# Kernel optimization log

Measured on AMD Instinct MI355X. Metric: run time of the kernel, lower is better.

Reference implementation:

```python
import jax, jax.numpy as jnp
import numpy as np

NMS_THRESHOLD = 0.4
TOP_K = 1000
MAX_BOXES = 300
N_ANCHORS = 300000
N_CLASSES = 80
DET_DIM = 85


def setup_inputs() -> dict:
    key = jax.random.key(0)
    k1, k2, k3, k4 = jax.random.split(key, 4)
    # valid [y1, x1, y2, x2] boxes: top-left corner + positive height/width
    yx = jax.random.uniform(k1, (1, N_ANCHORS, 2), jnp.float32) * 512.0
    hw = jax.random.uniform(k2, (1, N_ANCHORS, 2), jnp.float32) * 64.0 + 1.0
    boxes = jnp.concatenate([yx, yx + hw], axis=-1)
    classification = jax.random.uniform(k3, (1, N_ANCHORS, N_CLASSES), jnp.float32)
    detections = jax.random.normal(k4, (1, N_ANCHORS, DET_DIM), jnp.float32)
    return {"boxes": boxes, "classification": classification, "detections": detections}


def _iou_matrix(b):
    # b: [K, 4] as [y1, x1, y2, x2]
    y1, x1, y2, x2 = b[:, 0], b[:, 1], b[:, 2], b[:, 3]
    area = (y2 - y1) * (x2 - x1)
    ih = jnp.clip(jnp.minimum(y2[:, None], y2[None, :]) - jnp.maximum(y1[:, None], y1[None, :]), 0.0)
    iw = jnp.clip(jnp.minimum(x2[:, None], x2[None, :]) - jnp.maximum(x1[:, None], x1[None, :]), 0.0)
    inter = ih * iw
    return inter / (area[:, None] + area[None, :] - inter + 1e-8)


def _nms_forward(boxes, classification, detections):
    b = boxes[0]                      # [N, 4]
    cls = classification[0]           # [N, C]
    det = detections[0]               # [N, D]
    scores = jnp.max(cls, axis=1)     # [N]
    # pre-NMS top-k filter (lax.top_k returns scores sorted descending)
    _, idx = jax.lax.top_k(scores, TOP_K)
    b_k = b[idx]                      # [K, 4]
    det_k = det[idx]                  # [K, D]
    iou = _iou_matrix(b_k)            # [K, K]
    # greedy NMS over score-sorted candidates: keep box i iff no higher-scoring
    # kept box overlaps it above the threshold
    def step(keep, i):
        suppressed = jnp.any(keep & (iou[i] > NMS_THRESHOLD))
        return keep.at[i].set(~suppressed), None
    keep, _ = jax.lax.scan(step, jnp.zeros(TOP_K, dtype=bool), jnp.arange(TOP_K))
    # first MAX_BOXES kept candidates (in score order), zero-padded
    pos = jnp.where(keep, jnp.arange(TOP_K), TOP_K)
    pos = jnp.sort(pos)[:MAX_BOXES]
    valid = pos < TOP_K
    sel = det_k[jnp.minimum(pos, TOP_K - 1)]          # [MAX_BOXES, D]
    out = jnp.where(valid[:, None], sel, 0.0)
    return out[None]                   # [1, MAX_BOXES, D]


def reference(boxes, classification, detections):
    return _nms_forward(boxes, classification, detections)
```

## Files before the change

### kernel.cpp

```cpp
#include <hip/hip_runtime.h>
#include <stdint.h>

#define N_ANCH   300000
#define N_CLS    80
#define DET_DIM  85
#define TOPK     1000
#define MAXB     300
#define NMS_THR  0.4f
#define CAP      4096
#define NBH      32
#define N4       (N_ANCH / 4)
#define ITH      ((N4 + NBH*1024 - 1) / (NBH*1024))

#define OFF_SBITS   0
#define OFF_HA      300032
#define OFF_HB      304128
#define OFF_META    308224
#define OFF_CAND    308288
#define OFF_TOPK    316480
#define OFF_BOXK    317480
#define OFF_MASK    321480

__device__ __forceinline__ void gridbar(uint32_t* bar, uint32_t target) {
    __syncthreads();
    if (threadIdx.x == 0) {
        __threadfence();
        __hip_atomic_fetch_add(bar, 1u, __ATOMIC_ACQ_REL, __HIP_MEMORY_SCOPE_AGENT);
        while (__hip_atomic_load(bar, __ATOMIC_RELAXED, __HIP_MEMORY_SCOPE_AGENT) < target)
            __builtin_amdgcn_s_sleep(2);
        __threadfence();
    }
    __syncthreads();
}

__global__ __launch_bounds__(256) void k_scores(const float4* __restrict__ cls4,
                                                uint32_t* __restrict__ sbits,
                                                uint32_t* __restrict__ ha,
                                                uint32_t* __restrict__ hb,
                                                uint32_t* __restrict__ meta) {
    int tid = threadIdx.x;
    if (blockIdx.x == 0) {
        if (tid == 0) { meta[4] = 0; meta[8] = 0; }
        for (int i = tid; i < 4096; i += 256) { ha[i] = 0; hb[i] = 0; }
    }
    int wave = tid >> 6, lane = tid & 63, g = lane >> 2, q = lane & 3;
    int row = blockIdx.x * 64 + wave * 16 + g;
    if (row >= N_ANCH) return;
    const float4* rp = cls4 + (size_t)row * 20;
    float m = -1.0f;
    #pragma unroll
    for (int k = 0; k < 5; k++) {
        float4 v = rp[q + k * 4];
        m = fmaxf(m, fmaxf(fmaxf(v.x, v.y), fmaxf(v.z, v.w)));
    }
    m = fmaxf(m, __shfl_xor(m, 1));
    m = fmaxf(m, __shfl_xor(m, 2));
    if (q == 0) sbits[row] = __float_as_uint(m);
}

__device__ __forceinline__ void agg_add(uint32_t* h, uint32_t bin, bool valid) {
    int lane = threadIdx.x & 63;
    bool done = !valid;
    while (true) {
        unsigned long long rem = __ballot(!done);
        if (rem == 0ull) break;
        int leader = __ffsll((long long)rem) - 1;
        uint32_t lbin = __shfl(bin, leader);
        bool mine = (!done) && (bin == lbin);
        unsigned long long grp = __ballot(mine);
        if (lane == leader) atomicAdd(&h[lbin], (uint32_t)__popcll(grp));
        done = done || mine;
    }
}

__device__ __forceinline__ void findthr_core(const uint32_t c[4], uint32_t* wred,
                                             uint32_t K, uint32_t* res) {
    int tid = threadIdx.x, lane = tid & 63, wave = tid >> 6;
    uint32_t s = c[0] + c[1] + c[2] + c[3];
    uint32_t x = s;
    #pragma unroll
    for (int off = 1; off < 64; off <<= 1) {
        uint32_t v = __shfl_up(x, off);
        if (lane >= off) x += v;
    }
    if (lane == 63) wred[wave] = x;
    __syncthreads();
    if (wave == 0) {
        uint32_t w = (lane < 16) ? wred[lane] : 0u;
        #pragma unroll
        for (int off = 1; off < 16; off <<= 1) {
            uint32_t v = __shfl_up(w, off);
            if (lane >= off) w += v;
        }
        if (lane < 16) wred[lane] = w;
    }
    __syncthreads();
    uint32_t base = (wave == 0) ? 0u : wred[wave - 1];
    uint32_t incl = base + x, excl = incl - s;
    if (excl < K && incl >= K) {
        uint32_t run = excl;
        #pragma unroll
        for (int k = 0; k < 4; k++) {
            uint32_t nr = run + c[k];
            if (run < K && nr >= K) { res[0] = 4095 - (tid * 4 + k); res[1] = run; }
            run = nr;
        }
    }
    __syncthreads();
}

__device__ __forceinline__ float iou_f(float4 a, float4 b) {
    #pragma clang fp contract(off)
    float areaA = (a.z - a.x) * (a.w - a.y);
    float areaB = (b.z - b.x) * (b.w - b.y);
    float ih = fminf(a.z, b.z) - fmaxf(a.x, b.x); ih = fmaxf(ih, 0.0f);
    float iw = fminf(a.w, b.w) - fmaxf(a.y, b.y); iw = fmaxf(iw, 0.0f);
    float inter = ih * iw;
    float denom = (areaA + areaB - inter) + 1e-8f;
    return inter / denom;
}

__global__ __launch_bounds__(1024) void k_select(const uint4* __restrict__ sb4,
                                                 uint32_t* __restrict__ ha,
                                                 uint32_t* __restrict__ hb,
                                                 uint32_t* __restrict__ meta,
                                                 unsigned long long* __restrict__ cand,
                                                 uint32_t* __restrict__ topk,
                                                 const float4* __restrict__ boxes4,
                                                 float4* __restrict__ boxk,
                                                 unsigned long long* __restrict__ M,
                                                 const float* __restrict__ det,
                                                 float* __restrict__ out) {
    __shared__ __align__(16) uint32_t h[4096];
    __shared__ uint32_t wred[16];
    __shared__ uint32_t mr[2];
    __shared__ uint32_t wsum[16];
    __shared__ unsigned long long candS[CAP];
    __shared__ int keeplS[MAXB];
    __shared__ uint32_t topkS[TOPK];

    const int tid = threadIdx.x, wave = tid >> 6, lane = tid & 63;
    const int blk = blockIdx.x;
    uint32_t* bar = &meta[8];

    for (int i = tid; i < 4096; i += 1024) h[i] = 0;
    __syncthreads();
    for (int it = 0; it < ITH; it++) {
        int t4 = (it * NBH + blk) * 1024 + tid;
        bool v = t4 < N4;
        uint4 sv = v ? sb4[t4] : make_uint4(0, 0, 0, 0);
        agg_add(h, sv.x >> 20, v);
        agg_add(h, sv.y >> 20, v);
        agg_add(h, sv.z >> 20, v);
        agg_add(h, sv.w >> 20, v);
    }
    __syncthreads();
    for (int i = tid; i < 4096; i += 1024) { uint32_t v = h[i]; if (v) atomicAdd(&ha[i], v); }
    gridbar(bar, NBH * 1);

    uint32_t c[4];
    {
        uint4 q = ((const uint4*)ha)[1023 - tid];
        c[0] = q.w; c[1] = q.z; c[2] = q.y; c[3] = q.x;
    }
    findthr_core(c, wred, TOPK, mr);
    const uint32_t binA = mr[0], GA = mr[1];
    for (int i = tid; i < 4096; i += 1024) h[i] = 0;
    __syncthreads();
    for (int it = 0; it < ITH; it++) {
        int t4 = (it * NBH + blk) * 1024 + tid;
        if (t4 < N4) {
            uint4 sv = sb4[t4];
            if ((sv.x >> 20) == binA) atomicAdd(&h[(sv.x >> 8) & 0xFFFu], 1u);
            if ((sv.y >> 20) == binA) atomicAdd(&h[(sv.y >> 8) & 0xFFFu], 1u);
            if ((sv.z >> 20) == binA) atomicAdd(&h[(sv.z >> 8) & 0xFFFu], 1u);
            if ((sv.w >> 20) == binA) atomicAdd(&h[(sv.w >> 8) & 0xFFFu], 1u);
        }
    }
    __syncthreads();
    for (int i = tid; i < 4096; i += 1024) { uint32_t v = h[i]; if (v) atomicAdd(&hb[i], v); }
    gridbar(bar, NBH * 2);

    {
        uint4 q = ((const uint4*)hb)[1023 - tid];
        c[0] = q.w; c[1] = q.z; c[2] = q.y; c[3] = q.x;
    }
    findthr_core(c, wred, TOPK - GA, mr);
    const uint32_t T24 = (binA << 12) | mr[0];
    uint32_t cw = 0;
    for (int it = 0; it < ITH; it++) {
        int t4 = (it * NBH + blk) * 1024 + tid;
        bool v = t4 < N4;
        uint4 sv = v ? sb4[t4] : make_uint4(0, 0, 0, 0);
        uint32_t sl[4] = {sv.x, sv.y, sv.z, sv.w};
        #pragma unroll
        for (int s = 0; s < 4; s++) {
            bool m = v && ((sl[s] >> 8) >= T24);
            cw += (uint32_t)__popcll(__ballot(m));
        }
    }
    if (lane == 0) wsum[wave] = cw;
    __syncthreads();
    if (tid == 0) {
        uint32_t tot = 0;
        #pragma unroll
        for (int w = 0; w < 16; w++) tot += wsum[w];
        uint32_t base = atomicAdd(&meta[4], tot);
        uint32_t r = base;
        #pragma unroll
        for (int w = 0; w < 16; w++) { uint32_t c0 = wsum[w]; wsum[w] = r; r += c0; }
    }
    __syncthreads();
    uint32_t wbase = wsum[wave];
    for (int it = 0; it < ITH; it++) {
        int t4 = (it * NBH + blk) * 1024 + tid;
        bool v = t4 < N4;
        uint4 sv = v ? sb4[t4] : make_uint4(0, 0, 0, 0);
        uint32_t sl[4] = {sv.x, sv.y, sv.z, sv.w};
        #pragma unroll
        for (int s = 0; s < 4; s++) {
            uint32_t sb = sl[s];
            bool m = v && ((sb >> 8) >= T24);
            unsigned long long b = __ballot(m);
            if (m) {
                uint32_t p = wbase + (uint32_t)__popcll(b & ((1ull << lane) - 1ull));
                uint32_t idx = (uint32_t)(t4 * 4 + s);
                if (p < CAP) cand[p] = ((unsigned long long)sb << 32) | (uint32_t)(~idx);
            }
            wbase += (uint32_t)__popcll(b);
        }
    }
    gridbar(bar, NBH * 3);

    uint32_t C = meta[4]; if (C > CAP) C = CAP;
    uint32_t Cpad = (C + 63u) & ~63u;
    for (uint32_t t = tid; t < Cpad; t += 1024) candS[t] = (t < C) ? cand[t] : 0ull;
    __syncthreads();
    for (uint32_t i = (uint32_t)(blk * 16 + wave); i < C; i += NBH * 16) {
        unsigned long long my = candS[i];
        uint32_t r = 0;
        for (uint32_t j0 = 0; j0 < Cpad; j0 += 64) {
            unsigned long long vj = candS[j0 + lane];
            r += (uint32_t)__popcll(__ballot(vj > my));
        }
        if (r < TOPK && lane == 0) {
            uint32_t idx = ~(uint32_t)(my & 0xFFFFFFFFull);
            if (idx < N_ANCH) { topk[r] = idx; boxk[r] = boxes4[idx]; }
        }
    }
    gridbar(bar, NBH * 4);

    float4* bks = (float4*)h;
    for (int i = tid; i < TOPK; i += 1024) bks[i] = boxk[i];
    __syncthreads();
    for (int gw = blk * 16 + wave; gw < TOPK * 16; gw += NBH * 16) {
        int i = gw >> 4, w = gw & 15;
        int j = w * 64 + lane;
        float4 bi = bks[i];
        float4 bj = bks[j < TOPK ? j : 0];
        bool ok = (j < TOPK) && (iou_f(bi, bj) > NMS_THR);
        unsigned long long m = __ballot(ok);
        if (lane == 0) M[i * 16 + w] = m;
    }
    gridbar(bar, NBH * 5);

    if (blk != 0) return;
    for (int i = tid; i < TOPK; i += 1024) topkS[i] = topk[i];
    if (tid < 64) {
        unsigned long long keptArr[16];
        #pragma unroll
        for (int cc = 0; cc < 16; cc++) {
            int i = cc * 64 + lane;
            unsigned long long pre = 0ull, Mic = 0ull;
            if (i < TOPK) {
                #pragma unroll
                for (int w = 0; w < cc; w++) pre |= M[i * 16 + w] & keptArr[w];
                Mic = M[i * 16 + cc];
            }
            unsigned long long pre_mask = __ballot(pre != 0ull);
            unsigned long long kc = 0ull;
            const int lim = (cc == 15) ? (TOPK - 960) : 64;
            for (int k = 0; k < lim; k++) {
                unsigned long long b = __ballot(((Mic >> k) & 1ull) != 0ull);
                bool sup = (((pre_mask >> k) & 1ull) != 0ull) || ((b & kc) != 0ull);
                kc |= sup ? 0ull : (1ull << k);
            }
            keptArr[cc] = kc;
        }
        uint32_t pfxw[16];
        uint32_t run = 0;
        #pragma unroll
        for (int w = 0; w < 16; w++) { pfxw[w] = run; run += (uint32_t)__popcll(keptArr[w]); }
        int total = (int)run; if (total > MAXB) total = MAXB;
        for (int r = total + lane; r < MAXB; r += 64) keeplS[r] = -1;
        #pragma unroll
        for (int w = 0; w < 16; w++) {
            int i = w * 64 + lane;
            if (i < TOPK) {
                unsigned long long kw = keptArr[w];
                if ((kw >> lane) & 1ull) {
                    uint32_t rank = pfxw[w] + (uint32_t)__popcll(kw & ((1ull << lane) - 1ull));
                    if (rank < MAXB) keeplS[rank] = i;
                }
            }
        }
    }
    __syncthreads();
    for (int t = tid; t < MAXB * DET_DIM; t += 1024) {
        int r = t / DET_DIM, col = t - r * DET_DIM;
        int pos = keeplS[r];
        float v = 0.0f;
        if (pos >= 0) v = det[(size_t)topkS[pos] * DET_DIM + col];
        out[t] = v;
    }
}

extern "C" void kernel_launch(void* const* d_in, const int* in_sizes, int n_in,
                              void* d_out, int out_size, void* d_ws, size_t ws_size,
                              hipStream_t stream) {
    const float4* boxes4 = (const float4*)d_in[0];
    const float4* cls4   = (const float4*)d_in[1];
    const float*  det    = (const float*)d_in[2];
    float* out = (float*)d_out;
    uint32_t* ws = (uint32_t*)d_ws;

    uint32_t* sbits = ws + OFF_SBITS;
    uint32_t* ha    = ws + OFF_HA;
    uint32_t* hb    = ws + OFF_HB;
    uint32_t* meta  = ws + OFF_META;
    unsigned long long* cand = (unsigned long long*)(ws + OFF_CAND);
    uint32_t* topk  = ws + OFF_TOPK;
    float4*   boxk  = (float4*)(ws + OFF_BOXK);
    unsigned long long* M = (unsigned long long*)(ws + OFF_MASK);

    k_scores<<<(N_ANCH + 63) / 64, 256, 0, stream>>>(cls4, sbits, ha, hb, meta);
    k_select<<<NBH, 1024, 0, stream>>>((const uint4*)sbits, ha, hb, meta, cand, topk,
                                       boxes4, boxk, M, det, out);
}
```

Before: 274.4 us.

## Relax grid barriers, single-pass candidate compaction, LDS mask, parallel output gather

```diff
diff --git a/kernel.cpp b/kernel.cpp
--- a/kernel.cpp
+++ b/kernel.cpp
@@ -1,5 +1,7 @@
 #include <hip/hip_runtime.h>
 #include <stdint.h>
+
+typedef unsigned long long u64;
 
 #define N_ANCH   300000
 #define N_CLS    80
@@ -20,15 +22,41 @@
 #define OFF_TOPK    316480
 #define OFF_BOXK    317480
 #define OFF_MASK    321480
-
-__device__ __forceinline__ void gridbar(uint32_t* bar, uint32_t target) {
-    __syncthreads();
+#define OFF_KEEPL   353480
+
+__device__ __forceinline__ uint32_t ld_b32(const uint32_t* p) {
+    return __hip_atomic_load(p, __ATOMIC_RELAXED, __HIP_MEMORY_SCOPE_AGENT);
+}
+__device__ __forceinline__ u64 ld_b64(const u64* p) {
+    return __hip_atomic_load(p, __ATOMIC_RELAXED, __HIP_MEMORY_SCOPE_AGENT);
+}
+__device__ __forceinline__ void st_b32(uint32_t* p, uint32_t v) {
+    __hip_atomic_store(p, v, __ATOMIC_RELAXED, __HIP_MEMORY_SCOPE_AGENT);
+}
+__device__ __forceinline__ void st_b64(u64* p, u64 v) {
+    __hip_atomic_store(p, v, __ATOMIC_RELAXED, __HIP_MEMORY_SCOPE_AGENT);
+}
+__device__ __forceinline__ void st_f4(float4* p, float4 v) {
+    union { float4 f; u64 u[2]; } cv; cv.f = v;
+    u64* q = (u64*)p;
+    st_b64(q, cv.u[0]); st_b64(q + 1, cv.u[1]);
+}
+__device__ __forceinline__ float4 ld_f4(const float4* p) {
+    union { float4 f; u64 u[2]; } cv;
+    const u64* q = (const u64*)p;
+    cv.u[0] = ld_b64(q); cv.u[1] = ld_b64(q + 1);
+    return cv.f;
+}
+
+__device__ __forceinline__ void gb_arrive(uint32_t* bar) {
+    __syncthreads();
+    if (threadIdx.x == 0)
+        __hip_atomic_fetch_add(bar, 1u, __ATOMIC_RELAXED, __HIP_MEMORY_SCOPE_AGENT);
+}
+__device__ __forceinline__ void gb_wait(uint32_t* bar, uint32_t target) {
     if (threadIdx.x == 0) {
-        __threadfence();
-        __hip_atomic_fetch_add(bar, 1u, __ATOMIC_ACQ_REL, __HIP_MEMORY_SCOPE_AGENT);
         while (__hip_atomic_load(bar, __ATOMIC_RELAXED, __HIP_MEMORY_SCOPE_AGENT) < target)
-            __builtin_amdgcn_s_sleep(2);
-        __threadfence();
+            __builtin_amdgcn_s_sleep(1);
     }
     __syncthreads();
 }
@@ -109,39 +137,29 @@
     __syncthreads();
 }
 
-__device__ __forceinline__ float iou_f(float4 a, float4 b) {
-    #pragma clang fp contract(off)
-    float areaA = (a.z - a.x) * (a.w - a.y);
-    float areaB = (b.z - b.x) * (b.w - b.y);
-    float ih = fminf(a.z, b.z) - fmaxf(a.x, b.x); ih = fmaxf(ih, 0.0f);
-    float iw = fminf(a.w, b.w) - fmaxf(a.y, b.y); iw = fmaxf(iw, 0.0f);
-    float inter = ih * iw;
-    float denom = (areaA + areaB - inter) + 1e-8f;
-    return inter / denom;
-}
+#define MSW(i, w) ((i) * 16 + (((w) + (i)) & 15))
 
 __global__ __launch_bounds__(1024) void k_select(const uint4* __restrict__ sb4,
                                                  uint32_t* __restrict__ ha,
                                                  uint32_t* __restrict__ hb,
                                                  uint32_t* __restrict__ meta,
-                                                 unsigned long long* __restrict__ cand,
+                                                 u64* __restrict__ cand,
                                                  uint32_t* __restrict__ topk,
                                                  const float4* __restrict__ boxes4,
                                                  float4* __restrict__ boxk,
-                                                 unsigned long long* __restrict__ M,
+                                                 u64* __restrict__ M,
+                                                 uint32_t* __restrict__ keepl,
                                                  const float* __restrict__ det,
                                                  float* __restrict__ out) {
-    __shared__ __align__(16) uint32_t h[4096];
+    __shared__ __align__(16) u64 big[16000];
     __shared__ uint32_t wred[16];
     __shared__ uint32_t mr[2];
-    __shared__ uint32_t wsum[16];
-    __shared__ unsigned long long candS[CAP];
-    __shared__ int keeplS[MAXB];
-    __shared__ uint32_t topkS[TOPK];
+    __shared__ uint32_t kidS[MAXB];
 
     const int tid = threadIdx.x, wave = tid >> 6, lane = tid & 63;
     const int blk = blockIdx.x;
     uint32_t* bar = &meta[8];
+    uint32_t* h = (uint32_t*)big;
 
     for (int i = tid; i < 4096; i += 1024) h[i] = 0;
     __syncthreads();
@@ -156,12 +174,13 @@
     }
     __syncthreads();
     for (int i = tid; i < 4096; i += 1024) { uint32_t v = h[i]; if (v) atomicAdd(&ha[i], v); }
-    gridbar(bar, NBH * 1);
+    gb_arrive(bar); gb_wait(bar, NBH * 1);
 
     uint32_t c[4];
     {
-        uint4 q = ((const uint4*)ha)[1023 - tid];
-        c[0] = q.w; c[1] = q.z; c[2] = q.y; c[3] = q.x;
+        uint32_t* base = ha + 4u * (1023u - (uint32_t)tid);
+        c[0] = ld_b32(base + 3); c[1] = ld_b32(base + 2);
+        c[2] = ld_b32(base + 1); c[3] = ld_b32(base + 0);
     }
     findthr_core(c, wred, TOPK, mr);
     const uint32_t binA = mr[0], GA = mr[1];
@@ -179,39 +198,15 @@
     }
     __syncthreads();
     for (int i = tid; i < 4096; i += 1024) { uint32_t v = h[i]; if (v) atomicAdd(&hb[i], v); }
-    gridbar(bar, NBH * 2);
+    gb_arrive(bar); gb_wait(bar, NBH * 2);
 
     {
-        uint4 q = ((const uint4*)hb)[1023 - tid];
-        c[0] = q.w; c[1] = q.z; c[2] = q.y; c[3] = q.x;
+        uint32_t* base = hb + 4u * (1023u - (uint32_t)tid);
+        c[0] = ld_b32(base + 3); c[1] = ld_b32(base + 2);
+        c[2] = ld_b32(base + 1); c[3] = ld_b32(base + 0);
     }
     findthr_core(c, wred, TOPK - GA, mr);
     const uint32_t T24 = (binA << 12) | mr[0];
-    uint32_t cw = 0;
-    for (int it = 0; it < ITH; it++) {
-        int t4 = (it * NBH + blk) * 1024 + tid;
-        bool v = t4 < N4;
-        uint4 sv = v ? sb4[t4] : make_uint4(0, 0, 0, 0);
-        uint32_t sl[4] = {sv.x, sv.y, sv.z, sv.w};
-        #pragma unroll
-        for (int s = 0; s < 4; s++) {
-            bool m = v && ((sl[s] >> 8) >= T24);
-            cw += (uint32_t)__popcll(__ballot(m));
-        }
-    }
-    if (lane == 0) wsum[wave] = cw;
-    __syncthreads();
-    if (tid == 0) {
-        uint32_t tot = 0;
-        #pragma unroll
-        for (int w = 0; w < 16; w++) tot += wsum[w];
-        uint32_t base = atomicAdd(&meta[4], tot);
-        uint32_t r = base;
-        #pragma unroll
-        for (int w = 0; w < 16; w++) { uint32_t c0 = wsum[w]; wsum[w] = r; r += c0; }
-    }
-    __syncthreads();
-    uint32_t wbase = wsum[wave];
     for (int it = 0; it < ITH; it++) {
         int t4 = (it * NBH + blk) * 1024 + tid;
         bool v = t4 < N4;
@@ -222,95 +217,125 @@
             uint32_t sb = sl[s];
             bool m = v && ((sb >> 8) >= T24);
             unsigned long long b = __ballot(m);
-            if (m) {
-                uint32_t p = wbase + (uint32_t)__popcll(b & ((1ull << lane) - 1ull));
-                uint32_t idx = (uint32_t)(t4 * 4 + s);
-                if (p < CAP) cand[p] = ((unsigned long long)sb << 32) | (uint32_t)(~idx);
+            if (b) {
+                int leader = __ffsll((long long)b) - 1;
+                uint32_t base2 = 0;
+                if (lane == leader) base2 = atomicAdd(&meta[4], (uint32_t)__popcll(b));
+                base2 = __shfl(base2, leader);
+                if (m) {
+                    uint32_t p = base2 + (uint32_t)__popcll(b & ((1ull << lane) - 1ull));
+                    uint32_t idx = (uint32_t)(t4 * 4 + s);
+                    if (p < CAP) st_b64(&cand[p], ((u64)sb << 32) | (uint32_t)(~idx));
+                }
             }
-            wbase += (uint32_t)__popcll(b);
-        }
-    }
-    gridbar(bar, NBH * 3);
-
-    uint32_t C = meta[4]; if (C > CAP) C = CAP;
+        }
+    }
+    gb_arrive(bar); gb_wait(bar, NBH * 3);
+
+    u64* candS = big;
+    uint32_t C = ld_b32(&meta[4]); if (C > CAP) C = CAP;
     uint32_t Cpad = (C + 63u) & ~63u;
-    for (uint32_t t = tid; t < Cpad; t += 1024) candS[t] = (t < C) ? cand[t] : 0ull;
+    for (uint32_t t = tid; t < Cpad; t += 1024) candS[t] = (t < C) ? ld_b64(&cand[t]) : 0ull;
     __syncthreads();
     for (uint32_t i = (uint32_t)(blk * 16 + wave); i < C; i += NBH * 16) {
-        unsigned long long my = candS[i];
+        u64 my = candS[i];
         uint32_t r = 0;
-        for (uint32_t j0 = 0; j0 < Cpad; j0 += 64) {
-            unsigned long long vj = candS[j0 + lane];
-            r += (uint32_t)__popcll(__ballot(vj > my));
-        }
+        for (uint32_t j0 = 0; j0 < Cpad; j0 += 64)
+            r += (uint32_t)__popcll(__ballot(candS[j0 + lane] > my));
         if (r < TOPK && lane == 0) {
             uint32_t idx = ~(uint32_t)(my & 0xFFFFFFFFull);
-            if (idx < N_ANCH) { topk[r] = idx; boxk[r] = boxes4[idx]; }
-        }
-    }
-    gridbar(bar, NBH * 4);
-
-    float4* bks = (float4*)h;
-    for (int i = tid; i < TOPK; i += 1024) bks[i] = boxk[i];
+            if (idx < N_ANCH) { st_b32(&topk[r], idx); st_f4(&boxk[r], boxes4[idx]); }
+        }
+    }
+    gb_arrive(bar); gb_wait(bar, NBH * 4);
+
+    float4* bks  = (float4*)big;
+    float* areaS = (float*)((char*)big + 16000);
+    for (int i = tid; i < TOPK; i += 1024) {
+        float4 b = ld_f4(&boxk[i]);
+        bks[i] = b;
+        {
+            #pragma clang fp contract(off)
+            areaS[i] = (b.z - b.x) * (b.w - b.y);
+        }
+    }
     __syncthreads();
     for (int gw = blk * 16 + wave; gw < TOPK * 16; gw += NBH * 16) {
         int i = gw >> 4, w = gw & 15;
-        int j = w * 64 + lane;
-        float4 bi = bks[i];
-        float4 bj = bks[j < TOPK ? j : 0];
-        bool ok = (j < TOPK) && (iou_f(bi, bj) > NMS_THR);
+        int j = w * 64 + lane, jc = j < TOPK ? j : 0;
+        float4 bi = bks[i], bj = bks[jc];
+        bool ok;
+        {
+            #pragma clang fp contract(off)
+            float ih = fminf(bi.z, bj.z) - fmaxf(bi.x, bj.x); ih = fmaxf(ih, 0.0f);
+            float iw = fminf(bi.w, bj.w) - fmaxf(bi.y, bj.y); iw = fmaxf(iw, 0.0f);
+            float inter = ih * iw;
+            float denom = (areaS[i] + areaS[jc] - inter) + 1e-8f;
+            ok = (j < TOPK) && (inter / denom > NMS_THR);
+        }
         unsigned long long m = __ballot(ok);
-        if (lane == 0) M[i * 16 + w] = m;
-    }
-    gridbar(bar, NBH * 5);
-
-    if (blk != 0) return;
-    for (int i = tid; i < TOPK; i += 1024) topkS[i] = topk[i];
-    if (tid < 64) {
-        unsigned long long keptArr[16];
-        #pragma unroll
-        for (int cc = 0; cc < 16; cc++) {
-            int i = cc * 64 + lane;
-            unsigned long long pre = 0ull, Mic = 0ull;
-            if (i < TOPK) {
-                #pragma unroll
-                for (int w = 0; w < cc; w++) pre |= M[i * 16 + w] & keptArr[w];
-                Mic = M[i * 16 + cc];
+        if (lane == 0) st_b64(&M[i * 16 + w], m);
+    }
+    gb_arrive(bar);
+
+    if (blk == 0) {
+        gb_wait(bar, NBH * 5);
+        u64* MS = big;
+        for (int t = tid; t < TOPK * 16; t += 1024) {
+            int i = t >> 4, w = t & 15;
+            MS[MSW(i, w)] = ld_b64(&M[t]);
+        }
+        __syncthreads();
+        if (tid < 64) {
+            u64 keptArr[16];
+            #pragma unroll
+            for (int cc = 0; cc < 16; cc++) {
+                int i = cc * 64 + lane;
+                u64 pre = 0ull, Mic = 0ull;
+                if (i < TOPK) {
+                    #pragma unroll
+                    for (int w = 0; w < cc; w++) pre |= MS[MSW(i, w)] & keptArr[w];
+                    Mic = MS[MSW(i, cc)];
+                }
+                unsigned long long pre_mask = __ballot(pre != 0ull);
+                u64 kc = 0ull;
+                const int lim = (cc == 15) ? (TOPK - 960) : 64;
+                for (int k = 0; k < lim; k++) {
+                    unsigned long long b = __ballot(((Mic >> k) & 1ull) != 0ull);
+                    bool sup = (((pre_mask >> k) & 1ull) != 0ull) || ((b & kc) != 0ull);
+                    kc |= sup ? 0ull : (1ull << k);
+                }
+                keptArr[cc] = kc;
             }
-            unsigned long long pre_mask = __ballot(pre != 0ull);
-            unsigned long long kc = 0ull;
-            const int lim = (cc == 15) ? (TOPK - 960) : 64;
-            for (int k = 0; k < lim; k++) {
-                unsigned long long b = __ballot(((Mic >> k) & 1ull) != 0ull);
-                bool sup = (((pre_mask >> k) & 1ull) != 0ull) || ((b & kc) != 0ull);
-                kc |= sup ? 0ull : (1ull << k);
-            }
-            keptArr[cc] = kc;
-        }
-        uint32_t pfxw[16];
-        uint32_t run = 0;
-        #pragma unroll
-        for (int w = 0; w < 16; w++) { pfxw[w] = run; run += (uint32_t)__popcll(keptArr[w]); }
-        int total = (int)run; if (total > MAXB) total = MAXB;
-        for (int r = total + lane; r < MAXB; r += 64) keeplS[r] = -1;
-        #pragma unroll
-        for (int w = 0; w < 16; w++) {
-            int i = w * 64 + lane;
-            if (i < TOPK) {
-                unsigned long long kw = keptArr[w];
-                if ((kw >> lane) & 1ull) {
-                    uint32_t rank = pfxw[w] + (uint32_t)__popcll(kw & ((1ull << lane) - 1ull));
-                    if (rank < MAXB) keeplS[rank] = i;
+            uint32_t pfxw[16];
+            uint32_t run = 0;
+            #pragma unroll
+            for (int w = 0; w < 16; w++) { pfxw[w] = run; run += (uint32_t)__popcll(keptArr[w]); }
+            int total = (int)run; if (total > MAXB) total = MAXB;
+            for (int r = total + lane; r < MAXB; r += 64) st_b32(&keepl[r], 0xFFFFFFFFu);
+            #pragma unroll
+            for (int w = 0; w < 16; w++) {
+                int i = w * 64 + lane;
+                if (i < TOPK) {
+                    u64 kw = keptArr[w];
+                    if ((kw >> lane) & 1ull) {
+                        uint32_t rank = pfxw[w] + (uint32_t)__popcll(kw & ((1ull << lane) - 1ull));
+                        if (rank < MAXB) st_b32(&keepl[rank], ld_b32(&topk[i]));
+                    }
                 }
             }
         }
     }
-    __syncthreads();
-    for (int t = tid; t < MAXB * DET_DIM; t += 1024) {
+    gb_arrive(bar); gb_wait(bar, NBH * 6);
+
+    if (tid < MAXB) kidS[tid] = ld_b32(&keepl[tid]);
+    __syncthreads();
+    int t = blk * 1024 + tid;
+    if (t < MAXB * DET_DIM) {
         int r = t / DET_DIM, col = t - r * DET_DIM;
-        int pos = keeplS[r];
+        uint32_t src = kidS[r];
         float v = 0.0f;
-        if (pos >= 0) v = det[(size_t)topkS[pos] * DET_DIM + col];
+        if (src < N_ANCH) v = det[(size_t)src * DET_DIM + col];
         out[t] = v;
     }
 }
@@ -328,12 +353,13 @@
     uint32_t* ha    = ws + OFF_HA;
     uint32_t* hb    = ws + OFF_HB;
     uint32_t* meta  = ws + OFF_META;
-    unsigned long long* cand = (unsigned long long*)(ws + OFF_CAND);
+    u64*      cand  = (u64*)(ws + OFF_CAND);
     uint32_t* topk  = ws + OFF_TOPK;
     float4*   boxk  = (float4*)(ws + OFF_BOXK);
-    unsigned long long* M = (unsigned long long*)(ws + OFF_MASK);
+    u64*      M     = (u64*)(ws + OFF_MASK);
+    uint32_t* keepl = ws + OFF_KEEPL;
 
     k_scores<<<(N_ANCH + 63) / 64, 256, 0, stream>>>(cls4, sbits, ha, hb, meta);
     k_select<<<NBH, 1024, 0, stream>>>((const uint4*)sbits, ha, hb, meta, cand, topk,
-                                       boxes4, boxk, M, det, out);
-}
+                                       boxes4, boxk, M, keepl, det, out);
+}
```

Measured after the change: 273.7 us. About the same (-0.3%).
